# Optimization experiments

Measured on AMD Instinct MI355X. Metric: run time of the kernel, lower is better.

The kernel has to match this reference:

```python
import jax, jax.numpy as jnp
import numpy as np

B, T, D, H, L, F, V = 2, 512, 512, 8, 6, 2048, 32000
EPS = 1e-6


def _ln(x, g, b):
    m = x.mean(-1, keepdims=True)
    v = ((x - m) ** 2).mean(-1, keepdims=True)
    return (x - m) / jnp.sqrt(v + EPS) * g + b


def _mha(qx, kx, qkv_w, qkv_b, ow, ob, mask):
    # Wide heads: each head has dim D (Linear(D, H*D) projections, Linear(H*D, D) output).
    Bq, Tq, _ = qx.shape
    def proj(xx, w, bi):
        return (xx @ w + bi).reshape(Bq, Tq, H, D).transpose(0, 2, 1, 3)  # (B,H,T,D)
    q = proj(qx, qkv_w[0], qkv_b[0])
    k = proj(kx, qkv_w[1], qkv_b[1])
    v = proj(kx, qkv_w[2], qkv_b[2])
    s = jnp.einsum('bhqd,bhkd->bhqk', q, k) / jnp.sqrt(jnp.float32(D))
    if mask is not None:
        s = jnp.where(mask, s, -jnp.inf)
    w = jax.nn.softmax(s, axis=-1)
    o = jnp.einsum('bhqk,bhkd->bhqd', w, v).transpose(0, 2, 1, 3).reshape(Bq, Tq, H * D)
    return o @ ow + ob


def _pe(t, d):
    pos = jnp.arange(t, dtype=jnp.float32)[:, None]
    wl = jnp.exp(jnp.arange(0, d, 2, dtype=jnp.float32) / d * -jnp.log(10000.0))
    pe = jnp.zeros((t, d), dtype=jnp.float32)
    pe = pe.at[:, 0::2].set(jnp.sin(pos * wl))
    pe = pe.at[:, 1::2].set(jnp.cos(pos * wl))
    return pe


def _forward(x, y, enc_emb, dec_emb, enc_qkv_w, enc_qkv_b, enc_out_w, enc_out_b,
             enc_ln1_g, enc_ln1_b, enc_ff_w1, enc_ff_b1, enc_ff_w2, enc_ff_b2,
             enc_ln2_g, enc_ln2_b, dec_sa_qkv_w, dec_sa_qkv_b, dec_sa_out_w, dec_sa_out_b,
             dec_ln1_g, dec_ln1_b, dec_ca_qkv_w, dec_ca_qkv_b, dec_ca_out_w, dec_ca_out_b,
             dec_ln2_g, dec_ln2_b, dec_ff_w1, dec_ff_b1, dec_ff_w2, dec_ff_b2,
             dec_ln3_g, dec_ln3_b, head_w, head_b):
    pe = _pe(T, D)
    scale = jnp.sqrt(jnp.float32(D))
    # ---- encoder ----
    h = enc_emb[x] * scale + pe  # (B,T,D)
    for i in range(L):
        a = _mha(h, h, enc_qkv_w[i], enc_qkv_b[i], enc_out_w[i], enc_out_b[i], None)
        h = _ln(a + h, enc_ln1_g[i], enc_ln1_b[i])
        f = jax.nn.relu(h @ enc_ff_w1[i] + enc_ff_b1[i]) @ enc_ff_w2[i] + enc_ff_b2[i]
        h = _ln(f + h, enc_ln2_g[i], enc_ln2_b[i])
    # ---- decoder ----
    causal = jnp.tril(jnp.ones((T, T), dtype=bool))[None, None]  # (1,1,T,T)
    d = dec_emb[y] * scale + pe
    for i in range(L):
        a = _mha(d, d, dec_sa_qkv_w[i], dec_sa_qkv_b[i], dec_sa_out_w[i], dec_sa_out_b[i], causal)
        d = _ln(a + d, dec_ln1_g[i], dec_ln1_b[i])
        c = _mha(d, h, dec_ca_qkv_w[i], dec_ca_qkv_b[i], dec_ca_out_w[i], dec_ca_out_b[i], None)
        d = _ln(c + d, dec_ln2_g[i], dec_ln2_b[i])
        f = jax.nn.relu(d @ dec_ff_w1[i] + dec_ff_b1[i]) @ dec_ff_w2[i] + dec_ff_b2[i]
        d = _ln(f + d, dec_ln3_g[i], dec_ln3_b[i])
    return d @ head_w + head_b  # (B,T,V) logits


def setup_inputs() -> dict:
    key = jax.random.key(0)
    ks = iter(jax.random.split(key, 40))
    def nrm(shape):
        return jax.random.normal(next(ks), shape, dtype=jnp.float32) * 0.02
    HD = H * D
    return {
        'x': jax.random.randint(next(ks), (B, T), 0, V, dtype=jnp.int32),
        'y': jax.random.randint(next(ks), (B, T), 0, V, dtype=jnp.int32),
        'enc_emb': nrm((V, D)), 'dec_emb': nrm((V, D)),
        'enc_qkv_w': nrm((L, 3, D, HD)), 'enc_qkv_b': jnp.zeros((L, 3, HD)),
        'enc_out_w': nrm((L, HD, D)), 'enc_out_b': jnp.zeros((L, D)),
        'enc_ln1_g': jnp.ones((L, D)), 'enc_ln1_b': jnp.zeros((L, D)),
        'enc_ff_w1': nrm((L, D, F)), 'enc_ff_b1': jnp.zeros((L, F)),
        'enc_ff_w2': nrm((L, F, D)), 'enc_ff_b2': jnp.zeros((L, D)),
        'enc_ln2_g': jnp.ones((L, D)), 'enc_ln2_b': jnp.zeros((L, D)),
        'dec_sa_qkv_w': nrm((L, 3, D, HD)), 'dec_sa_qkv_b': jnp.zeros((L, 3, HD)),
        'dec_sa_out_w': nrm((L, HD, D)), 'dec_sa_out_b': jnp.zeros((L, D)),
        'dec_ln1_g': jnp.ones((L, D)), 'dec_ln1_b': jnp.zeros((L, D)),
        'dec_ca_qkv_w': nrm((L, 3, D, HD)), 'dec_ca_qkv_b': jnp.zeros((L, 3, HD)),
        'dec_ca_out_w': nrm((L, HD, D)), 'dec_ca_out_b': jnp.zeros((L, D)),
        'dec_ln2_g': jnp.ones((L, D)), 'dec_ln2_b': jnp.zeros((L, D)),
        'dec_ff_w1': nrm((L, D, F)), 'dec_ff_b1': jnp.zeros((L, F)),
        'dec_ff_w2': nrm((L, F, D)), 'dec_ff_b2': jnp.zeros((L, D)),
        'dec_ln3_g': jnp.ones((L, D)), 'dec_ln3_b': jnp.zeros((L, D)),
        'head_w': nrm((D, V)), 'head_b': jnp.zeros((V,)),
    }


def reference(x, y, enc_emb, dec_emb, enc_qkv_w, enc_qkv_b, enc_out_w, enc_out_b,
              enc_ln1_g, enc_ln1_b, enc_ff_w1, enc_ff_b1, enc_ff_w2, enc_ff_b2,
              enc_ln2_g, enc_ln2_b, dec_sa_qkv_w, dec_sa_qkv_b, dec_sa_out_w, dec_sa_out_b,
              dec_ln1_g, dec_ln1_b, dec_ca_qkv_w, dec_ca_qkv_b, dec_ca_out_w, dec_ca_out_b,
              dec_ln2_g, dec_ln2_b, dec_ff_w1, dec_ff_b1, dec_ff_w2, dec_ff_b2,
              dec_ln3_g, dec_ln3_b, head_w, head_b):
    return _forward(x, y, enc_emb, dec_emb, enc_qkv_w, enc_qkv_b, enc_out_w, enc_out_b,
                    enc_ln1_g, enc_ln1_b, enc_ff_w1, enc_ff_b1, enc_ff_w2, enc_ff_b2,
                    enc_ln2_g, enc_ln2_b, dec_sa_qkv_w, dec_sa_qkv_b, dec_sa_out_w, dec_sa_out_b,
                    dec_ln1_g, dec_ln1_b, dec_ca_qkv_w, dec_ca_qkv_b, dec_ca_out_w, dec_ca_out_b,
                    dec_ln2_g, dec_ln2_b, dec_ff_w1, dec_ff_b1, dec_ff_w2, dec_ff_b2,
                    dec_ln3_g, dec_ln3_b, head_w, head_b)
```

## Files before the change

kernel.cpp:

```cpp
#include <hip/hip_runtime.h>
#include <hip/hip_bf16.h>

#define B_ 2
#define T_ 512
#define D_ 512
#define H_ 8
#define L_ 6
#define F_ 2048
#define V_ 32000
#define BT_ (B_ * T_)
#define HD_ (H_ * D_)
#define BH_ (B_ * H_)

typedef __attribute__((ext_vector_type(8))) short short8;
typedef __attribute__((ext_vector_type(4))) short short4v;
typedef __attribute__((ext_vector_type(4))) float f32x4;

__device__ __forceinline__ short f2b(float f) {
  __hip_bfloat16 h = __float2bfloat16(f);
  short u; __builtin_memcpy(&u, &h, 2); return u;
}
__device__ __forceinline__ void store_c(float* p, float v) { *p = v; }
__device__ __forceinline__ void store_c(short* p, float v) { *p = f2b(v); }

__global__ __launch_bounds__(256) void embed_kernel(
    const int* __restrict__ tok, const float* __restrict__ emb,
    float* __restrict__ out, short* __restrict__ out16)
{
  const int row = blockIdx.x;
  const int t = row & (T_ - 1);
  const int token = tok[row];
  const float* e = emb + (size_t)token * D_;
  float* o = out + (size_t)row * D_;
  short* o16 = out16 + (size_t)row * D_;
  const float scale = sqrtf((float)D_);
  const float nl = -logf(10000.0f);
  for (int d = threadIdx.x; d < D_; d += 256) {
    int i = d >> 1;
    float wl = expf(nl * (2.0f * (float)i) / (float)D_);
    float ang = (float)t * wl;
    float pe = (d & 1) ? cosf(ang) : sinf(ang);
    float v = e[d] * scale + pe;
    o[d] = v; o16[d] = f2b(v);
  }
}

template<bool BTM, typename OutT, int BM>
__global__ __launch_bounds__(256, BM == 128 ? 2 : 3) void mfma_gemm(
    const short* __restrict__ A, long lda, long a_hi, long a_lo,
    const void* __restrict__ Bv, long ldb, long b_hi, long b_lo,
    OutT* __restrict__ C, long ldc, long c_hi, long c_lo, long pstride,
    short* __restrict__ Ct, int trans_hh, int relu,
    int K, int nh, int ksplit, float scale,
    const float* __restrict__ bias, long bias_stride)
{
  constexpr int SA = BM + 1;
  constexpr int AU = BM / 32;
  constexpr int WRN = (BM == 128) ? 2 : 1;
  constexpr int WN  = (BM == 128) ? 64 : 32;
  constexpr int NR  = WN / 16;
  __shared__ short8 As8[2 * 8 * SA];
  __shared__ short8 Bs8[2 * 8 * 129];
  const int tid = threadIdx.x;
  const int bh = blockIdx.z / ksplit;
  const int kz = blockIdx.z - bh * ksplit;
  const int bb = bh / nh, hh = bh - bb * nh;
  const short* Ab = A + (long)bb * a_hi + (long)hh * a_lo;
  const short* Bbs = (const short*)Bv + (long)bb * b_hi + (long)hh * b_lo;
  const float* Bbf = (const float*)Bv + (long)bb * b_hi + (long)hh * b_lo;
  OutT* Cb = C + (long)bb * c_hi + (long)hh * c_lo + (long)kz * pstride;

  const int gx = gridDim.x, gy = gridDim.y;
  const int nwg = gx * gy;
  int lin = blockIdx.y * gx + blockIdx.x;
  {
    const int xcd = lin & 7, idx = lin >> 3;
    const int q = nwg >> 3, r = nwg & 7;
    lin = (xcd < r ? xcd * (q + 1) : r * (q + 1) + (xcd - r) * q) + idx;
  }
  const int bn = (lin / gy) * 128;
  const int bm = (lin % gy) * BM;

  const int klen = K / ksplit, kbase = kz * klen;
  const int lane = tid & 63, wid = tid >> 6;
  const int wr = (WRN == 2) ? (wid >> 1) : 0;
  const int wc = (WRN == 2) ? (wid & 1) : wid;
  const int lg = lane >> 4, r16 = lane & 15;

  int arow[AU], acol[AU];
#pragma unroll
  for (int u = 0; u < AU; ++u) { int o = u * 256 + tid; arow[u] = o >> 3; acol[u] = o & 7; }
  int brow[4], bcol[4];
#pragma unroll
  for (int u = 0; u < 4; ++u) { int o = u * 256 + tid; brow[u] = o >> 3; bcol[u] = o & 7; }
  const int ncol = tid & 127, nsh = tid >> 7;

  short8 pa0[AU], pa1[AU];
  short8 pbt0[4], pbt1[4];
  float  pbn0[4][8], pbn1[4][8];

#define LOADSET(PA, PBT, PBN, K0)                                               \
  {                                                                             \
    _Pragma("unroll")                                                           \
    for (int u = 0; u < AU; ++u)                                                \
      PA[u] = *(const short8*)(Ab + (long)(bm + arow[u]) * lda + ((K0) + acol[u] * 8)); \
    if constexpr (BTM) {                                                        \
      _Pragma("unroll")                                                         \
      for (int u = 0; u < 4; ++u)                                               \
        PBT[u] = *(const short8*)(Bbs + (long)(bn + brow[u]) * ldb + ((K0) + bcol[u] * 8)); \
    } else {                                                                    \
      const float* s_ = Bbf + (long)((K0) + nsh * 32) * ldb + (bn + ncol);      \
      _Pragma("unroll")                                                         \
      for (int i = 0; i < 4; ++i)                                               \
        _Pragma("unroll")                                                       \
        for (int j = 0; j < 8; ++j)                                             \
          PBN[i][j] = s_[(long)(i * 8 + j) * ldb];                              \
    }                                                                           \
  }

#define STAGESET(PA, PBT, PBN, BUF)                                             \
  {                                                                             \
    const int ao_ = (BUF) * 8 * SA, bo_ = (BUF) * 8 * 129;                      \
    _Pragma("unroll")                                                           \
    for (int u = 0; u < AU; ++u) As8[ao_ + acol[u] * SA + arow[u]] = PA[u];     \
    if constexpr (BTM) {                                                        \
      _Pragma("unroll")                                                         \
      for (int u = 0; u < 4; ++u) Bs8[bo_ + bcol[u] * 129 + brow[u]] = PBT[u];  \
    } else {                                                                    \
      _Pragma("unroll")                                                         \
      for (int i = 0; i < 4; ++i) {                                             \
        short8 v_;                                                              \
        _Pragma("unroll")                                                       \
        for (int j = 0; j < 8; ++j) v_[j] = f2b(PBN[i][j]);                     \
        Bs8[bo_ + (nsh * 4 + i) * 129 + ncol] = v_;                             \
      }                                                                         \
    }                                                                           \
  }

  f32x4 acc[4][NR] = {};
  auto domfma = [&](int buf) {
    const int ao = buf * 8 * SA, bo = buf * 8 * 129;
#pragma unroll
    for (int kb = 0; kb < 2; ++kb) {
      const int cha = ao + (kb * 4 + lg) * SA;
      const int chb = bo + (kb * 4 + lg) * 129;
      short8 a0 = As8[cha + wr * 64 +  0 + r16];
      short8 a1 = As8[cha + wr * 64 + 16 + r16];
      short8 a2 = As8[cha + wr * 64 + 32 + r16];
      short8 a3 = As8[cha + wr * 64 + 48 + r16];
#pragma unroll
      for (int n = 0; n < NR; ++n) {
        short8 bfr = Bs8[chb + wc * WN + n * 16 + r16];
        acc[0][n] = __builtin_amdgcn_mfma_f32_16x16x32_bf16(a0, bfr, acc[0][n], 0, 0, 0);
        acc[1][n] = __builtin_amdgcn_mfma_f32_16x16x32_bf16(a1, bfr, acc[1][n], 0, 0, 0);
        acc[2][n] = __builtin_amdgcn_mfma_f32_16x16x32_bf16(a2, bfr, acc[2][n], 0, 0, 0);
        acc[3][n] = __builtin_amdgcn_mfma_f32_16x16x32_bf16(a3, bfr, acc[3][n], 0, 0, 0);
      }
    }
  };

  const int nsteps = klen >> 6;
  LOADSET(pa0, pbt0, pbn0, kbase)
  STAGESET(pa0, pbt0, pbn0, 0)
  if (nsteps > 1) LOADSET(pa1, pbt1, pbn1, kbase + 64)
  __syncthreads();

  for (int t = 0; t + 1 < nsteps; t += 2) {
    if (t + 2 < nsteps) LOADSET(pa0, pbt0, pbn0, kbase + (t + 2) * 64)
    domfma(0);
    STAGESET(pa1, pbt1, pbn1, 1)
    __syncthreads();
    if (t + 3 < nsteps) LOADSET(pa1, pbt1, pbn1, kbase + (t + 3) * 64)
    domfma(1);
    if (t + 2 < nsteps) {
      STAGESET(pa0, pbt0, pbn0, 0)
      __syncthreads();
    }
  }
#undef LOADSET
#undef STAGESET

  const float* bp = bias ? bias + (long)hh * bias_stride : nullptr;
  if (hh == trans_hh) {
#pragma unroll
    for (int m = 0; m < 4; ++m)
#pragma unroll
      for (int n = 0; n < NR; ++n) {
        const int col = bn + wc * WN + n * 16 + r16;
        const float badd = bp ? bp[col] : 0.0f;
        short4v sv;
#pragma unroll
        for (int rr = 0; rr < 4; ++rr) sv[rr] = f2b(acc[m][n][rr] * scale + badd);
        *(short4v*)(Ct + (long)col * BT_ + (bm + wr * 64 + m * 16 + lg * 4)) = sv;
      }
  } else {
#pragma unroll
    for (int m = 0; m < 4; ++m)
#pragma unroll
      for (int rr = 0; rr < 4; ++rr) {
        const int row = bm + wr * 64 + m * 16 + lg * 4 + rr;
        OutT* crow = Cb + (long)row * ldc + bn + wc * WN + r16;
#pragma unroll
        for (int n = 0; n < NR; ++n) {
          float v = acc[m][n][rr] * scale;
          if (bp) v += bp[bn + wc * WN + n * 16 + r16];
          if (relu) v = fmaxf(v, 0.0f);
          store_c(&crow[n * 16], v);
        }
      }
  }
}

__global__ __launch_bounds__(256) void reduce_ln_kernel(
    const float* __restrict__ P, long pstride, int ks,
    const float* __restrict__ bias, float* __restrict__ hbuf, short* __restrict__ h16,
    const float* __restrict__ gam, const float* __restrict__ bet)
{
  __shared__ float red[256];
  const int row = blockIdx.x, tid = threadIdx.x;
  const long base = (long)row * D_;
  float s0 = hbuf[base + tid] + bias[tid];
  float s1 = hbuf[base + tid + 256] + bias[tid + 256];
  for (int z = 0; z < ks; ++z) {
    s0 += P[(long)z * pstride + base + tid];
    s1 += P[(long)z * pstride + base + tid + 256];
  }
  red[tid] = s0 + s1; __syncthreads();
  for (int o = 128; o > 0; o >>= 1) { if (tid < o) red[tid] += red[tid + o]; __syncthreads(); }
  const float mean = red[0] * (1.0f / D_); __syncthreads();
  const float d0 = s0 - mean, d1 = s1 - mean;
  red[tid] = d0 * d0 + d1 * d1; __syncthreads();
  for (int o = 128; o > 0; o >>= 1) { if (tid < o) red[tid] += red[tid + o]; __syncthreads(); }
  const float inv = rsqrtf(red[0] * (1.0f / D_) + 1e-6f);
  const float v0 = d0 * inv * gam[tid] + bet[tid];
  const float v1 = d1 * inv * gam[tid + 256] + bet[tid + 256];
  hbuf[base + tid] = v0;       h16[base + tid] = f2b(v0);
  hbuf[base + tid + 256] = v1; h16[base + tid + 256] = f2b(v1);
}

__global__ __launch_bounds__(256) void softmax_kernel(
    const float* __restrict__ S, short* __restrict__ P, int causal)
{
  __shared__ float red[256];
  const int q = blockIdx.x, bh = blockIdx.y, tid = threadIdx.x;
  const float* row = S + ((size_t)bh * T_ + q) * T_;
  short* prow = P + ((size_t)bh * T_ + q) * T_;
  const int n = causal ? (q + 1) : T_;
  const float v0 = row[tid], v1 = row[tid + 256];
  const bool in0 = tid < n, in1 = (tid + 256) < n;
  red[tid] = fmaxf(in0 ? v0 : -3.0e38f, in1 ? v1 : -3.0e38f);
  __syncthreads();
  for (int o = 128; o > 0; o >>= 1) { if (tid < o) red[tid] = fmaxf(red[tid], red[tid + o]); __syncthreads(); }
  const float m = red[0]; __syncthreads();
  const float e0 = in0 ? expf(v0 - m) : 0.0f;
  const float e1 = in1 ? expf(v1 - m) : 0.0f;
  red[tid] = e0 + e1; __syncthreads();
  for (int o = 128; o > 0; o >>= 1) { if (tid < o) red[tid] += red[tid + o]; __syncthreads(); }
  const float inv = 1.0f / red[0];
  prow[tid] = f2b(e0 * inv);
  prow[tid + 256] = f2b(e1 * inv);
}

extern "C" void kernel_launch(void* const* d_in, const int* in_sizes, int n_in,
                              void* d_out, int out_size, void* d_ws, size_t ws_size,
                              hipStream_t stream)
{
  const int*   x         = (const int*)d_in[0];
  const int*   y         = (const int*)d_in[1];
  const float* enc_emb   = (const float*)d_in[2];
  const float* dec_emb   = (const float*)d_in[3];
  const float* enc_qkv_w = (const float*)d_in[4];
  const float* enc_qkv_b = (const float*)d_in[5];
  const float* enc_out_w = (const float*)d_in[6];
  const float* enc_out_b = (const float*)d_in[7];
  const float* enc_ln1_g = (const float*)d_in[8];
  const float* enc_ln1_b = (const float*)d_in[9];
  const float* enc_ff_w1 = (const float*)d_in[10];
  const float* enc_ff_b1 = (const float*)d_in[11];
  const float* enc_ff_w2 = (const float*)d_in[12];
  const float* enc_ff_b2 = (const float*)d_in[13];
  const float* enc_ln2_g = (const float*)d_in[14];
  const float* enc_ln2_b = (const float*)d_in[15];
  const float* dec_sa_qkv_w = (const float*)d_in[16];
  const float* dec_sa_qkv_b = (const float*)d_in[17];
  const float* dec_sa_out_w = (const float*)d_in[18];
  const float* dec_sa_out_b = (const float*)d_in[19];
  const float* dec_ln1_g = (const float*)d_in[20];
  const float* dec_ln1_b = (const float*)d_in[21];
  const float* dec_ca_qkv_w = (const float*)d_in[22];
  const float* dec_ca_qkv_b = (const float*)d_in[23];
  const float* dec_ca_out_w = (const float*)d_in[24];
  const float* dec_ca_out_b = (const float*)d_in[25];
  const float* dec_ln2_g = (const float*)d_in[26];
  const float* dec_ln2_b = (const float*)d_in[27];
  const float* dec_ff_w1 = (const float*)d_in[28];
  const float* dec_ff_b1 = (const float*)d_in[29];
  const float* dec_ff_w2 = (const float*)d_in[30];
  const float* dec_ff_b2 = (const float*)d_in[31];
  const float* dec_ln3_g = (const float*)d_in[32];
  const float* dec_ln3_b = (const float*)d_in[33];
  const float* head_w    = (const float*)d_in[34];
  const float* head_b    = (const float*)d_in[35];
  float* out = (float*)d_out;

  char* wsb = (char*)d_ws;
  size_t off = 0;
  auto carve = [&](size_t bytes) { char* p = wsb + off; off += (bytes + 255) & ~255ull; return p; };
  float* h    = (float*)carve((size_t)BT_ * D_ * 4);
  float* dd   = (float*)carve((size_t)BT_ * D_ * 4);
  short* hb16 = (short*)carve((size_t)BT_ * D_ * 2);
  short* db16 = (short*)carve((size_t)BT_ * D_ * 2);
  short* Qb   = (short*)carve((size_t)BT_ * HD_ * 2);
  short* Kb   = (short*)carve((size_t)BT_ * HD_ * 2);
  short* Vt   = (short*)carve((size_t)HD_ * BT_ * 2);
  float* Sb   = (float*)carve((size_t)BH_ * T_ * T_ * 4);
  short* Pb   = (short*)carve((size_t)BH_ * T_ * T_ * 2);
  short* Ob   = Qb;
  short* mid  = Qb;
  (void)ws_size;

  dim3 blk(256);
  const long TT  = (long)T_ * T_;
  const long THD = (long)T_ * HD_;
  const long WQKV = (long)D_ * HD_;

  auto gemm = [&](bool bt, bool of32, bool bm64, int relu,
                  const short* A, long lda, long a_hi, long a_lo,
                  const void* Bp, long ldb, long b_hi, long b_lo,
                  void* Cp, long ldc, long c_hi, long c_lo, long pstride,
                  short* Ct, int trans_hh,
                  int M, int N, int K, int batch, int nh, int ksplit,
                  float scale, const float* bias, long bstride) {
    dim3 grd(N / 128, M / (bm64 ? 64 : 128), batch * ksplit);
    if (bm64) {
      if (bt) {
        if (of32) mfma_gemm<true , float, 64><<<grd, blk, 0, stream>>>(A, lda, a_hi, a_lo, Bp, ldb, b_hi, b_lo,
            (float*)Cp, ldc, c_hi, c_lo, pstride, Ct, trans_hh, relu, K, nh, ksplit, scale, bias, bstride);
        else      mfma_gemm<true , short, 64><<<grd, blk, 0, stream>>>(A, lda, a_hi, a_lo, Bp, ldb, b_hi, b_lo,
            (short*)Cp, ldc, c_hi, c_lo, pstride, Ct, trans_hh, relu, K, nh, ksplit, scale, bias, bstride);
      } else {
        if (of32) mfma_gemm<false, float, 64><<<grd, blk, 0, stream>>>(A, lda, a_hi, a_lo, Bp, ldb, b_hi, b_lo,
            (float*)Cp, ldc, c_hi, c_lo, pstride, Ct, trans_hh, relu, K, nh, ksplit, scale, bias, bstride);
        else      mfma_gemm<false, short, 64><<<grd, blk, 0, stream>>>(A, lda, a_hi, a_lo, Bp, ldb, b_hi, b_lo,
            (short*)Cp, ldc, c_hi, c_lo, pstride, Ct, trans_hh, relu, K, nh, ksplit, scale, bias, bstride);
      }
    } else {
      if (bt) {
        if (of32) mfma_gemm<true , float, 128><<<grd, blk, 0, stream>>>(A, lda, a_hi, a_lo, Bp, ldb, b_hi, b_lo,
            (float*)Cp, ldc, c_hi, c_lo, pstride, Ct, trans_hh, relu, K, nh, ksplit, scale, bias, bstride);
        else      mfma_gemm<true , short, 128><<<grd, blk, 0, stream>>>(A, lda, a_hi, a_lo, Bp, ldb, b_hi, b_lo,
            (short*)Cp, ldc, c_hi, c_lo, pstride, Ct, trans_hh, relu, K, nh, ksplit, scale, bias, bstride);
      } else {
        if (of32) mfma_gemm<false, float, 128><<<grd, blk, 0, stream>>>(A, lda, a_hi, a_lo, Bp, ldb, b_hi, b_lo,
            (float*)Cp, ldc, c_hi, c_lo, pstride, Ct, trans_hh, relu, K, nh, ksplit, scale, bias, bstride);
        else      mfma_gemm<false, short, 128><<<grd, blk, 0, stream>>>(A, lda, a_hi, a_lo, Bp, ldb, b_hi, b_lo,
            (short*)Cp, ldc, c_hi, c_lo, pstride, Ct, trans_hh, relu, K, nh, ksplit, scale, bias, bstride);
      }
    }
  };

  auto attention = [&](const short* qsrc, const short* kvsrc, bool self,
                       const float* qkvw, const float* qkvb,
                       const float* ow, const float* ob,
                       float* resid, short* resid16, int causal,
                       const float* lng, const float* lnb) {
    if (self) {
      gemm(false, false, false, 0, qsrc, D_, 0, 0, qkvw, HD_, 0, WQKV,
           Qb, HD_, 0, (long)(Kb - Qb), 0, Vt, 2,
           BT_, HD_, D_, 3, 3, 1, 1.0f, qkvb, HD_);
    } else {
      gemm(false, false, false, 0, qsrc, D_, 0, 0, qkvw, HD_, 0, 0,
           Qb, HD_, 0, 0, 0, nullptr, -1,
           BT_, HD_, D_, 1, 1, 1, 1.0f, qkvb, 0);
      gemm(false, false, false, 0, kvsrc, D_, 0, 0, qkvw + WQKV, HD_, 0, WQKV,
           Kb, HD_, 0, 0, 0, Vt, 1,
           BT_, HD_, D_, 2, 2, 1, 1.0f, qkvb + HD_, HD_);
    }
    gemm(true, true, false, 0, Qb, HD_, THD, D_, Kb, HD_, THD, D_,
         Sb, T_, (long)H_ * TT, TT, 0, nullptr, -1,
         T_, T_, D_, BH_, H_, 1, 0.044194173824159216f, nullptr, 0);
    softmax_kernel<<<dim3(T_, BH_), blk, 0, stream>>>(Sb, Pb, causal);
    gemm(true, false, false, 0, Pb, T_, (long)H_ * TT, TT, Vt, BT_, T_, (long)D_ * BT_,
         Ob, HD_, THD, D_, 0, nullptr, -1,
         T_, D_, T_, BH_, H_, 1, 1.0f, nullptr, 0);
    gemm(false, true, false, 0, Ob, HD_, 0, 0, ow, D_, 0, 0,
         Sb, D_, 0, 0, (long)BT_ * D_, nullptr, -1,
         BT_, D_, HD_, 1, 1, 8, 1.0f, nullptr, 0);
    reduce_ln_kernel<<<dim3(BT_), blk, 0, stream>>>(
        Sb, (long)BT_ * D_, 8, ob, resid, resid16, lng, lnb);
  };

  auto ffn = [&](float* resid, short* resid16,
                 const float* w1, const float* b1,
                 const float* w2, const float* b2,
                 const float* lng, const float* lnb) {
    gemm(false, false, true, 1, resid16, D_, 0, 0, w1, F_, 0, 0,
         mid, F_, 0, 0, 0, nullptr, -1,
         BT_, F_, D_, 1, 1, 1, 1.0f, b1, 0);
    gemm(false, true, false, 0, mid, F_, 0, 0, w2, D_, 0, 0,
         Sb, D_, 0, 0, (long)BT_ * D_, nullptr, -1,
         BT_, D_, F_, 1, 1, 8, 1.0f, nullptr, 0);
    reduce_ln_kernel<<<dim3(BT_), blk, 0, stream>>>(
        Sb, (long)BT_ * D_, 8, b2, resid, resid16, lng, lnb);
  };

  embed_kernel<<<dim3(BT_), blk, 0, stream>>>(x, enc_emb, h, hb16);
  for (int i = 0; i < L_; ++i) {
    attention(hb16, hb16, true,
              enc_qkv_w + (size_t)i * 3 * WQKV, enc_qkv_b + (size_t)i * 3 * HD_,
              enc_out_w + (size_t)i * HD_ * D_, enc_out_b + (size_t)i * D_,
              h, hb16, 0, enc_ln1_g + (size_t)i * D_, enc_ln1_b + (size_t)i * D_);
    ffn(h, hb16, enc_ff_w1 + (size_t)i * D_ * F_, enc_ff_b1 + (size_t)i * F_,
        enc_ff_w2 + (size_t)i * F_ * D_, enc_ff_b2 + (size_t)i * D_,
        enc_ln2_g + (size_t)i * D_, enc_ln2_b + (size_t)i * D_);
  }

  embed_kernel<<<dim3(BT_), blk, 0, stream>>>(y, dec_emb, dd, db16);
  for (int i = 0; i < L_; ++i) {
    attention(db16, db16, true,
              dec_sa_qkv_w + (size_t)i * 3 * WQKV, dec_sa_qkv_b + (size_t)i * 3 * HD_,
              dec_sa_out_w + (size_t)i * HD_ * D_, dec_sa_out_b + (size_t)i * D_,
              dd, db16, 1, dec_ln1_g + (size_t)i * D_, dec_ln1_b + (size_t)i * D_);
    attention(db16, hb16, false,
              dec_ca_qkv_w + (size_t)i * 3 * WQKV, dec_ca_qkv_b + (size_t)i * 3 * HD_,
              dec_ca_out_w + (size_t)i * HD_ * D_, dec_ca_out_b + (size_t)i * D_,
              dd, db16, 0, dec_ln2_g + (size_t)i * D_, dec_ln2_b + (size_t)i * D_);
    ffn(dd, db16, dec_ff_w1 + (size_t)i * D_ * F_, dec_ff_b1 + (size_t)i * F_,
        dec_ff_w2 + (size_t)i * F_ * D_, dec_ff_b2 + (size_t)i * D_,
        dec_ln3_g + (size_t)i * D_, dec_ln3_b + (size_t)i * D_);
  }

  gemm(false, true, false, 0, db16, D_, 0, 0, head_w, V_, 0, 0,
       out, V_, 0, 0, 0, nullptr, -1,
       BT_, V_, D_, 1, 1, 1, 1.0f, head_b, 0);
}
```

Before: 2.465 ms.

## Fuse QK^T, softmax and PV into a single flash-attention kernel

Replaces the score GEMM, the standalone softmax kernel and the PV GEMM with one online-softmax attention kernel. Each block handles 32 query rows of one head; its four waves split the 512-wide head dimension and sum partial scores through LDS. Causal blocks skip key tiles above the diagonal. This removes the fp32 score buffer and the bf16 probability buffer, along with their global write and read traffic and two kernel launches. In exchange the kernel uses small 32x32 tiles, several block barriers per key tile, only 256 blocks per call, uneven work across causal blocks, and it writes O in place over the Q buffer.

Result: slower. 3.491 ms (+41.6%).

```diff
diff --git a/kernel.cpp b/kernel.cpp
--- a/kernel.cpp
+++ b/kernel.cpp
@@ -211,6 +211,142 @@
   }
 }
 
+__global__ __launch_bounds__(256, 3) void flash_attn_kernel(
+    const short* Q, const short* __restrict__ Kg,
+    const short* __restrict__ Vtg, short* O, int causal)
+{
+  __shared__ short8 KV[4 * 528];
+  __shared__ float Sred[4][32][33];
+  __shared__ short8 Pl[4 * 33];
+  __shared__ float rowm[32], rowl[32], rowf[32];
+
+  const int tid = threadIdx.x;
+  const int lane = tid & 63, w = tid >> 6;
+  const int lg = lane >> 4, r16 = lane & 15;
+
+  const int lin = blockIdx.y + blockIdx.z * (T_ / 32);
+  const int xcd = lin & 7, rr_ = lin >> 3;
+  const int qi = rr_ & 15, hi = rr_ >> 4;
+  const int bh = xcd * 2 + hi;
+  const int b = bh >> 3, hh = bh & 7;
+  const int q0 = qi * 32;
+  const int dc = w * 128;
+
+  const short* Qbase = Q + ((long)b * T_ + q0) * HD_ + hh * D_ + dc;
+  const short* Kbase = Kg + ((long)b * T_) * HD_ + hh * D_ + dc;
+  const short* Vbase = Vtg + ((long)(hh * D_ + dc)) * BT_ + (long)b * T_;
+  short8* KVw = KV + w * 528;
+
+  short8 qf[2][4];
+#pragma unroll
+  for (int rg = 0; rg < 2; ++rg)
+#pragma unroll
+    for (int ks = 0; ks < 4; ++ks)
+      qf[rg][ks] = *(const short8*)(Qbase + (long)(rg * 16 + r16) * HD_ + ks * 32 + lg * 8);
+
+  f32x4 o[2][8] = {};
+  if (tid < 32) { rowm[tid] = -3.0e38f; rowl[tid] = 0.0f; }
+
+  const int nkv = causal ? (q0 / 32 + 1) : (T_ / 32);
+  const float sscale = 0.044194173824159216f;
+
+  for (int kt = 0; kt < nkv; ++kt) {
+    __syncthreads();
+#pragma unroll
+    for (int i = 0; i < 8; ++i) {
+      int idx = i * 64 + lane;
+      int tok = idx >> 4, oct = idx & 15;
+      KVw[oct * 33 + tok] = *(const short8*)(Kbase + (long)(kt * 32 + tok) * HD_ + oct * 8);
+    }
+    __syncthreads();
+    f32x4 s[2][2] = {};
+#pragma unroll
+    for (int ks = 0; ks < 4; ++ks) {
+#pragma unroll
+      for (int ng = 0; ng < 2; ++ng) {
+        short8 kb = KVw[(ks * 4 + lg) * 33 + ng * 16 + r16];
+        s[0][ng] = __builtin_amdgcn_mfma_f32_16x16x32_bf16(qf[0][ks], kb, s[0][ng], 0, 0, 0);
+        s[1][ng] = __builtin_amdgcn_mfma_f32_16x16x32_bf16(qf[1][ks], kb, s[1][ng], 0, 0, 0);
+      }
+    }
+#pragma unroll
+    for (int rg = 0; rg < 2; ++rg)
+#pragma unroll
+      for (int ng = 0; ng < 2; ++ng)
+#pragma unroll
+        for (int rr = 0; rr < 4; ++rr)
+          Sred[w][rg * 16 + lg * 4 + rr][ng * 16 + r16] = s[rg][ng][rr];
+    __syncthreads();
+#pragma unroll
+    for (int i = 0; i < 8; ++i) {
+      int idx = i * 64 + lane;
+      int d = idx & 127, oct = idx >> 7;
+      KVw[oct * 129 + d] = *(const short8*)(Vbase + (long)d * BT_ + kt * 32 + oct * 8);
+    }
+    {
+      const int row = tid >> 3, sub = tid & 7;
+      const int kvb = sub * 4;
+      float v0 = Sred[0][row][kvb+0] + Sred[1][row][kvb+0] + Sred[2][row][kvb+0] + Sred[3][row][kvb+0];
+      float v1 = Sred[0][row][kvb+1] + Sred[1][row][kvb+1] + Sred[2][row][kvb+1] + Sred[3][row][kvb+1];
+      float v2 = Sred[0][row][kvb+2] + Sred[1][row][kvb+2] + Sred[2][row][kvb+2] + Sred[3][row][kvb+2];
+      float v3 = Sred[0][row][kvb+3] + Sred[1][row][kvb+3] + Sred[2][row][kvb+3] + Sred[3][row][kvb+3];
+      v0 *= sscale; v1 *= sscale; v2 *= sscale; v3 *= sscale;
+      if (causal) {
+        const int qg = q0 + row, kg = kt * 32 + kvb;
+        if (kg + 0 > qg) v0 = -3.0e38f;
+        if (kg + 1 > qg) v1 = -3.0e38f;
+        if (kg + 2 > qg) v2 = -3.0e38f;
+        if (kg + 3 > qg) v3 = -3.0e38f;
+      }
+      float mx = fmaxf(fmaxf(v0, v1), fmaxf(v2, v3));
+      mx = fmaxf(mx, __shfl_xor(mx, 1));
+      mx = fmaxf(mx, __shfl_xor(mx, 2));
+      mx = fmaxf(mx, __shfl_xor(mx, 4));
+      const float mo = rowm[row];
+      const float mn = fmaxf(mo, mx);
+      const float p0 = expf(v0 - mn), p1 = expf(v1 - mn);
+      const float p2 = expf(v2 - mn), p3 = expf(v3 - mn);
+      float sm = p0 + p1 + p2 + p3;
+      sm += __shfl_xor(sm, 1);
+      sm += __shfl_xor(sm, 2);
+      sm += __shfl_xor(sm, 4);
+      const float f = expf(mo - mn);
+      if (sub == 0) { rowl[row] = rowl[row] * f + sm; rowm[row] = mn; rowf[row] = f; }
+      short* Pls = (short*)Pl;
+      const int oct = sub >> 1;
+      short4v pv;
+      pv[0] = f2b(p0); pv[1] = f2b(p1); pv[2] = f2b(p2); pv[3] = f2b(p3);
+      *(short4v*)(Pls + ((long)(oct * 33) + row) * 8 + (sub & 1) * 4) = pv;
+    }
+    __syncthreads();
+#pragma unroll
+    for (int rg = 0; rg < 2; ++rg) {
+      const float f0 = rowf[rg * 16 + lg * 4 + 0];
+      const float f1 = rowf[rg * 16 + lg * 4 + 1];
+      const float f2 = rowf[rg * 16 + lg * 4 + 2];
+      const float f3 = rowf[rg * 16 + lg * 4 + 3];
+      short8 a = Pl[lg * 33 + rg * 16 + r16];
+#pragma unroll
+      for (int ng = 0; ng < 8; ++ng) {
+        o[rg][ng][0] *= f0; o[rg][ng][1] *= f1; o[rg][ng][2] *= f2; o[rg][ng][3] *= f3;
+        short8 vb = KVw[lg * 129 + ng * 16 + r16];
+        o[rg][ng] = __builtin_amdgcn_mfma_f32_16x16x32_bf16(a, vb, o[rg][ng], 0, 0, 0);
+      }
+    }
+  }
+  short* Obase = O + ((long)b * T_ + q0) * HD_ + hh * D_ + dc;
+#pragma unroll
+  for (int rg = 0; rg < 2; ++rg)
+#pragma unroll
+    for (int rr = 0; rr < 4; ++rr) {
+      const int row = rg * 16 + lg * 4 + rr;
+      const float inv = 1.0f / rowl[row];
+#pragma unroll
+      for (int ng = 0; ng < 8; ++ng)
+        Obase[(long)row * HD_ + ng * 16 + r16] = f2b(o[rg][ng][rr] * inv);
+    }
+}
+
 __global__ __launch_bounds__(256) void reduce_ln_kernel(
     const float* __restrict__ P, long pstride, int ks,
     const float* __restrict__ bias, float* __restrict__ hbuf, short* __restrict__ h16,
@@ -236,29 +372,6 @@
   const float v1 = d1 * inv * gam[tid + 256] + bet[tid + 256];
   hbuf[base + tid] = v0;       h16[base + tid] = f2b(v0);
   hbuf[base + tid + 256] = v1; h16[base + tid + 256] = f2b(v1);
-}
-
-__global__ __launch_bounds__(256) void softmax_kernel(
-    const float* __restrict__ S, short* __restrict__ P, int causal)
-{
-  __shared__ float red[256];
-  const int q = blockIdx.x, bh = blockIdx.y, tid = threadIdx.x;
-  const float* row = S + ((size_t)bh * T_ + q) * T_;
-  short* prow = P + ((size_t)bh * T_ + q) * T_;
-  const int n = causal ? (q + 1) : T_;
-  const float v0 = row[tid], v1 = row[tid + 256];
-  const bool in0 = tid < n, in1 = (tid + 256) < n;
-  red[tid] = fmaxf(in0 ? v0 : -3.0e38f, in1 ? v1 : -3.0e38f);
-  __syncthreads();
-  for (int o = 128; o > 0; o >>= 1) { if (tid < o) red[tid] = fmaxf(red[tid], red[tid + o]); __syncthreads(); }
-  const float m = red[0]; __syncthreads();
-  const float e0 = in0 ? expf(v0 - m) : 0.0f;
-  const float e1 = in1 ? expf(v1 - m) : 0.0f;
-  red[tid] = e0 + e1; __syncthreads();
-  for (int o = 128; o > 0; o >>= 1) { if (tid < o) red[tid] += red[tid + o]; __syncthreads(); }
-  const float inv = 1.0f / red[0];
-  prow[tid] = f2b(e0 * inv);
-  prow[tid + 256] = f2b(e1 * inv);
 }
 
 extern "C" void kernel_launch(void* const* d_in, const int* in_sizes, int n_in,
@@ -314,13 +427,11 @@
   short* Kb   = (short*)carve((size_t)BT_ * HD_ * 2);
   short* Vt   = (short*)carve((size_t)HD_ * BT_ * 2);
   float* Sb   = (float*)carve((size_t)BH_ * T_ * T_ * 4);
-  short* Pb   = (short*)carve((size_t)BH_ * T_ * T_ * 2);
   short* Ob   = Qb;
   short* mid  = Qb;
   (void)ws_size;
 
   dim3 blk(256);
-  const long TT  = (long)T_ * T_;
   const long THD = (long)T_ * HD_;
   const long WQKV = (long)D_ * HD_;
 
@@ -345,17 +456,10 @@
             (short*)Cp, ldc, c_hi, c_lo, pstride, Ct, trans_hh, relu, K, nh, ksplit, scale, bias, bstride);
       }
     } else {
-      if (bt) {
-        if (of32) mfma_gemm<true , float, 128><<<grd, blk, 0, stream>>>(A, lda, a_hi, a_lo, Bp, ldb, b_hi, b_lo,
-            (float*)Cp, ldc, c_hi, c_lo, pstride, Ct, trans_hh, relu, K, nh, ksplit, scale, bias, bstride);
-        else      mfma_gemm<true , short, 128><<<grd, blk, 0, stream>>>(A, lda, a_hi, a_lo, Bp, ldb, b_hi, b_lo,
-            (short*)Cp, ldc, c_hi, c_lo, pstride, Ct, trans_hh, relu, K, nh, ksplit, scale, bias, bstride);
-      } else {
-        if (of32) mfma_gemm<false, float, 128><<<grd, blk, 0, stream>>>(A, lda, a_hi, a_lo, Bp, ldb, b_hi, b_lo,
-            (float*)Cp, ldc, c_hi, c_lo, pstride, Ct, trans_hh, relu, K, nh, ksplit, scale, bias, bstride);
-        else      mfma_gemm<false, short, 128><<<grd, blk, 0, stream>>>(A, lda, a_hi, a_lo, Bp, ldb, b_hi, b_lo,
-            (short*)Cp, ldc, c_hi, c_lo, pstride, Ct, trans_hh, relu, K, nh, ksplit, scale, bias, bstride);
-      }
+      if (of32) mfma_gemm<false, float, 128><<<grd, blk, 0, stream>>>(A, lda, a_hi, a_lo, Bp, ldb, b_hi, b_lo,
+          (float*)Cp, ldc, c_hi, c_lo, pstride, Ct, trans_hh, relu, K, nh, ksplit, scale, bias, bstride);
+      else      mfma_gemm<false, short, 128><<<grd, blk, 0, stream>>>(A, lda, a_hi, a_lo, Bp, ldb, b_hi, b_lo,
+          (short*)Cp, ldc, c_hi, c_lo, pstride, Ct, trans_hh, relu, K, nh, ksplit, scale, bias, bstride);
     }
   };
 
@@ -376,13 +480,7 @@
            Kb, HD_, 0, 0, 0, Vt, 1,
            BT_, HD_, D_, 2, 2, 1, 1.0f, qkvb + HD_, HD_);
     }
-    gemm(true, true, false, 0, Qb, HD_, THD, D_, Kb, HD_, THD, D_,
-         Sb, T_, (long)H_ * TT, TT, 0, nullptr, -1,
-         T_, T_, D_, BH_, H_, 1, 0.044194173824159216f, nullptr, 0);
-    softmax_kernel<<<dim3(T_, BH_), blk, 0, stream>>>(Sb, Pb, causal);
-    gemm(true, false, false, 0, Pb, T_, (long)H_ * TT, TT, Vt, BT_, T_, (long)D_ * BT_,
-         Ob, HD_, THD, D_, 0, nullptr, -1,
-         T_, D_, T_, BH_, H_, 1, 1.0f, nullptr, 0);
+    flash_attn_kernel<<<dim3(1, T_ / 32, BH_), blk, 0, stream>>>(Qb, Kb, Vt, Ob, causal);
     gemm(false, true, false, 0, Ob, HD_, 0, 0, ow, D_, 0, 0,
          Sb, D_, 0, 0, (long)BT_ * D_, nullptr, -1,
          BT_, D_, HD_, 1, 1, 8, 1.0f, nullptr, 0);
```
